# Performance work log

Hardware: AMD Instinct MI355X
Metric: run time of the kernel (lower is better)

The kernel has to match this reference:

```python
import jax, jax.numpy as jnp
import numpy as np
import math

B, T, E = 2, 2048, 1024
H = 16
D = E // H  # head_dim = 64

def setup_inputs() -> dict:
    key = jax.random.key(0)
    k1, k2, k3, k4, k5 = jax.random.split(key, 5)
    s = 0.02
    return {
        "x": jax.random.normal(k1, (B, T, E), dtype=jnp.float32),
        "W_attn": jax.random.normal(k2, (E, 3 * E), dtype=jnp.float32) * s,
        "b_attn": jax.random.normal(k3, (3 * E,), dtype=jnp.float32) * s,
        "W_proj": jax.random.normal(k4, (E, E), dtype=jnp.float32) * s,
        "b_proj": jax.random.normal(k5, (E,), dtype=jnp.float32) * s,
    }

def reference(x, W_attn, b_attn, W_proj, b_proj):
    Bx, Tx, Ex = x.shape
    qkv = x @ W_attn + b_attn                      # [B,T,3E]
    q, k, v = jnp.split(qkv, 3, axis=2)
    # [B,T,E] -> [B,H,T,D]
    def heads(t):
        return t.reshape(Bx, Tx, H, D).transpose(0, 2, 1, 3)
    q, k, v = heads(q), heads(k), heads(v)
    scores = jnp.einsum('bhqd,bhkd->bhqk', q, k) / math.sqrt(D)
    causal = jnp.tril(jnp.ones((Tx, Tx), dtype=bool))
    scores = jnp.where(causal, scores, -jnp.inf)
    attn = jax.nn.softmax(scores, axis=-1)
    out = jnp.einsum('bhqk,bhkd->bhqd', attn, v)   # [B,H,T,D]
    out = out.transpose(0, 2, 1, 3).reshape(Bx, Tx, Ex)
    return out @ W_proj + b_proj
```

## Files before the change

kernel.cpp:

```cpp
#include <hip/hip_runtime.h>


typedef unsigned short u16;
typedef unsigned int u32;
typedef __bf16 bf8 __attribute__((ext_vector_type(8)));
typedef float f32x4 __attribute__((ext_vector_type(4)));
typedef float f32x16 __attribute__((ext_vector_type(16)));
typedef u32 u32x4v __attribute__((ext_vector_type(4)));

__device__ __forceinline__ u16 f2b(float f) {
    return __builtin_bit_cast(u16, (__bf16)f);
}

__device__ __forceinline__ u32 pk2(float lo, float hi) {
    return (u32)f2b(lo) | ((u32)f2b(hi) << 16);
}

__device__ __forceinline__ f32x4 mfma16(bf8 a, bf8 b, f32x4 c) {
    return __builtin_amdgcn_mfma_f32_16x16x32_bf16(a, b, c, 0, 0, 0);
}

__device__ __forceinline__ f32x16 mfma32(bf8 a, bf8 b, f32x16 c) {
    return __builtin_amdgcn_mfma_f32_32x32x16_bf16(a, b, c, 0, 0, 0);
}

__device__ __forceinline__ float fexp2(float x) {
    return __builtin_amdgcn_exp2f(x);
}

__device__ __forceinline__ void pl32swap(u32& a, u32& b) {
    asm("v_permlane32_swap_b32 %0, %1" : "+v"(a), "+v"(b));
}

__device__ __forceinline__ void gload_lds16(const u16* g, u16* l) {
    __builtin_amdgcn_global_load_lds(
        (__attribute__((address_space(1))) void*)(g),
        (__attribute__((address_space(3))) void*)(l), 16, 0, 0);
}

__global__ __launch_bounds__(256) void k_prep(const float* __restrict__ x,
                                              const float* __restrict__ Wa,
                                              const float* __restrict__ Wp,
                                              u16* __restrict__ Xb,
                                              u16* __restrict__ WtA,
                                              u16* __restrict__ WtP) {
    __shared__ float tile[64][65];
    int id = blockIdx.x, t = threadIdx.x;
    if (id < 4096) {
        int i = id * 256 + t;
        float4 v = ((const float4*)x)[i];
        ushort4 o;
        o.x = f2b(v.x); o.y = f2b(v.y); o.z = f2b(v.z); o.w = f2b(v.w);
        ((ushort4*)Xb)[i] = o;
        return;
    }
    const float* in; u16* out; int N, j;
    if (id < 4864) { j = id - 4096; in = Wa; out = WtA; N = 3072; }
    else           { j = id - 4864; in = Wp; out = WtP; N = 1024; }
    int k0 = (j & 15) * 64, n0 = (j >> 4) * 64;
    int c = t & 63, r0 = t >> 6;
#pragma unroll
    for (int i = 0; i < 16; ++i) {
        int r = r0 + i * 4;
        tile[r][c] = in[(size_t)(k0 + r) * N + n0 + c];
    }
    __syncthreads();
#pragma unroll
    for (int i = 0; i < 16; ++i) {
        int r = r0 + i * 4;
        out[(size_t)(n0 + r) * 1024 + k0 + c] = f2b(tile[c][r]);
    }
}

#define GEMM_STAGE(GA0, GA1, GB0, GB1, K, B)                                   \
    do {                                                                       \
        gload_lds16(GA0 + (K), As[B] + tid * 8);                               \
        gload_lds16(GA1 + (K), As[B] + (256 + tid) * 8);                       \
        gload_lds16(GB0 + (K), Bs[B] + tid * 8);                               \
        gload_lds16(GB1 + (K), Bs[B] + (256 + tid) * 8);                       \
    } while (0)

#define GEMM_CORE(Aptr, Bptr)                                                  \
    int tid = threadIdx.x;                                                     \
    int w = tid >> 6, lane = tid & 63, l16 = lane & 15, quad = lane >> 4;      \
    int m0 = blockIdx.x * 128, n0 = blockIdx.y * 128;                          \
    int wr = (w >> 1) * 64, wc = (w & 1) * 64;                                 \
    __shared__ u16 As[2][128 * 32];                                            \
    __shared__ u16 Bs[2][128 * 32];                                            \
    f32x4 acc[4][4];                                                           \
    _Pragma("unroll") for (int mi = 0; mi < 4; ++mi)                           \
        _Pragma("unroll") for (int ni = 0; ni < 4; ++ni)                       \
            _Pragma("unroll") for (int r = 0; r < 4; ++r) acc[mi][ni][r] = 0.f;\
    int srow0 = tid >> 2, srow1 = 64 + srow0;                                  \
    int slc = ((tid & 3) ^ ((tid >> 3) & 3)) * 8;      \
    const u16* gA0 = Aptr + (size_t)(m0 + srow0) * 1024 + slc;                 \
    const u16* gA1 = Aptr + (size_t)(m0 + srow1) * 1024 + slc;                 \
    const u16* gB0 = Bptr + (size_t)(n0 + srow0) * 1024 + slc;                 \
    const u16* gB1 = Bptr + (size_t)(n0 + srow1) * 1024 + slc;                 \
    int cq = (quad ^ ((l16 >> 1) & 3)) * 8;               \
    GEMM_STAGE(gA0, gA1, gB0, gB1, 0, 0);                                      \
    for (int it = 0; it < 32; ++it) {                                          \
        int pb = it & 1;                                                       \
        __syncthreads();                           \
        bf8 af[4], bf[4];                                                      \
        _Pragma("unroll") for (int mi = 0; mi < 4; ++mi)                       \
            af[mi] = *(const bf8*)(As[pb] + (wr + mi * 16 + l16) * 32 + cq);   \
        _Pragma("unroll") for (int ni = 0; ni < 4; ++ni)                       \
            bf[ni] = *(const bf8*)(Bs[pb] + (wc + ni * 16 + l16) * 32 + cq);   \
        if (it < 31) GEMM_STAGE(gA0, gA1, gB0, gB1, (it + 1) * 32, pb ^ 1);    \
        _Pragma("unroll") for (int mi = 0; mi < 4; ++mi)                       \
            _Pragma("unroll") for (int ni = 0; ni < 4; ++ni)                   \
                acc[mi][ni] = mfma16(af[mi], bf[ni], acc[mi][ni]);             \
    }

__global__ __launch_bounds__(256, 3) void k_qkv(const u16* __restrict__ Xb,
                                                const u16* __restrict__ WtA,
                                                const float* __restrict__ ba,
                                                u16* __restrict__ Qb,
                                                u16* __restrict__ Kb,
                                                u16* __restrict__ Vtb) {
    GEMM_CORE(Xb, WtA)
    int sel = n0 >> 10;
    u16* dst = sel == 0 ? Qb : (sel == 1 ? Kb : Vtb);
    const float qs = 0.18033688011112042f;
#pragma unroll
    for (int ni = 0; ni < 4; ++ni) {
        int n = n0 + wc + ni * 16 + l16;
        float bias = ba[n];
        int h = (n & 1023) >> 6;
        int d = n & 63;
#pragma unroll
        for (int mi = 0; mi < 4; ++mi)
#pragma unroll
            for (int r = 0; r < 4; ++r) {
                int m = m0 + wr + mi * 16 + quad * 4 + r;
                int bb = m >> 11, tt = m & 2047;
                float v = acc[mi][ni][r] + bias;
                size_t hb = (size_t)(bb * 16 + h);
                if (sel == 2)
                    dst[hb * 131072 + (size_t)(tt >> 6) * 4096 + d * 64 + (tt & 63)] = f2b(v);
                else
                    dst[(hb * 2048 + tt) * 64 + d] =
                        f2b(sel == 0 ? v * qs : v);
            }
    }
}

__global__ __launch_bounds__(256, 3) void k_proj(const u16* __restrict__ AO,
                                                 const u16* __restrict__ WtP,
                                                 const float* __restrict__ bp,
                                                 float* __restrict__ out) {
    GEMM_CORE(AO, WtP)
#pragma unroll
    for (int ni = 0; ni < 4; ++ni) {
        int n = n0 + wc + ni * 16 + l16;
        float bias = bp[n];
#pragma unroll
        for (int mi = 0; mi < 4; ++mi)
#pragma unroll
            for (int r = 0; r < 4; ++r) {
                int m = m0 + wr + mi * 16 + quad * 4 + r;
                out[(size_t)m * 1024 + n] = acc[mi][ni][r] + bias;
            }
    }
}


#define STAGE128(KT2, B) do {                                                 \
    const u16* kt_ = Kh + (size_t)(KT2) * 8192;                               \
    const u16* vt_ = Vh + (size_t)(KT2) * 8192;                               \
    _Pragma("unroll") for (int i_ = 0; i_ < 2; ++i_) {                        \
        int ci_ = i_ * 512 + tid;             \
        gload_lds16(kt_ + (ci_ >> 3) * 64 +                                   \
                    (((ci_ & 7) ^ ((ci_ >> 3) & 7)) * 8),                     \
                    SMEM[B][0] + ci_ * 8);                                    \
        gload_lds16(vt_ + (ci_ >> 3) * 64 +                                   \
                    (((ci_ & 7) ^ ((ci_ >> 3) & 7)) * 8),                     \
                    SMEM[B][1] + ci_ * 8);                                    \
    }                                                                         \
} while (0)

#define PVSTEP(SG, BFR) do {                                                  \
    bf8 va_ = *(const bf8*)(vb_ + l31 * 64 + (((2 * (SG) + h) ^ swz) * 8));   \
    bf8 vc_ = *(const bf8*)(vb_ + (32 + l31) * 64 +                           \
                            (((2 * (SG) + h) ^ swz) * 8));                    \
    bf8 pf_ = __builtin_bit_cast(bf8, BFR);                                   \
    oT0 = mfma32(va_, pf_, oT0);                                              \
    oT1 = mfma32(vc_, pf_, oT1);                                              \
} while (0)

#define REPACK_PV(ST, SG0, SG1) do {                                          \
    u32 pk_[8];                                                               \
    _Pragma("unroll") for (int j = 0; j < 8; ++j)                             \
        pk_[j] = pk2(ST[2 * j], ST[2 * j + 1]);                               \
    pl32swap(pk_[0], pk_[2]); pl32swap(pk_[1], pk_[3]);                       \
    pl32swap(pk_[4], pk_[6]); pl32swap(pk_[5], pk_[7]);                       \
    u32x4v f0_ = {pk_[0], pk_[1], pk_[2], pk_[3]};                            \
    u32x4v f1_ = {pk_[4], pk_[5], pk_[6], pk_[7]};                            \
    PVSTEP(SG0, f0_);                                                         \
    PVSTEP(SG1, f1_);                                                         \
} while (0)

#define TREE16(S)                                                             \
    (((((S)[0] + (S)[1]) + ((S)[2] + (S)[3])) +                               \
      (((S)[4] + (S)[5]) + ((S)[6] + (S)[7]))) +                              \
     ((((S)[8] + (S)[9]) + ((S)[10] + (S)[11])) +                             \
      (((S)[12] + (S)[13]) + ((S)[14] + (S)[15]))))

__global__ __launch_bounds__(512, 4) void k_attn(const u16* __restrict__ Qb,
                                                 const u16* __restrict__ Kb,
                                                 const u16* __restrict__ Vtb,
                                                 u16* __restrict__ AO) {
    int id = blockIdx.x;
    int bh = (id & 7) * 4 + ((id >> 3) & 3);
    int t  = 15 - (id >> 5);
    int tid = threadIdx.x;
    int w = tid >> 6, lane = tid & 63, l31 = lane & 31, h = lane >> 5;
    int wq = w & 3, p = w >> 2;

    const u16* Qh = Qb  + (size_t)bh * 131072;
    const u16* Kh = Kb  + (size_t)bh * 131072;
    const u16* Vh = Vtb + (size_t)bh * 131072;

    __shared__ u16 SMEM[2][2][8192];

    int tq = 4 * t + wq;
    int qr = tq * 32;
    int ktmax = tq >> 1;
    int nk2 = t + 1;

    bf8 qf[4];
#pragma unroll
    for (int s = 0; s < 4; ++s)
        qf[s] = *(const bf8*)(Qh + (size_t)(qr + l31) * 64 + s * 16 + h * 8);

    float l_acc = 0.f;
    f32x16 oT0, oT1;
#pragma unroll
    for (int r = 0; r < 16; ++r) { oT0[r] = 0.f; oT1[r] = 0.f; }

    int swz = l31 & 7;

    STAGE128(0, 0);
    for (int k2 = 0; k2 < nk2; ++k2) {
        int pb = k2 & 1;
        __syncthreads();
        if (k2 + 1 < nk2) STAGE128(k2 + 1, pb ^ 1);

        int kt = 2 * k2 + p;
        if (kt <= ktmax) {
            const u16* kb_ = SMEM[pb][0] + p * 4096;
            const u16* vb_ = SMEM[pb][1] + p * 4096;
            bool diag = (kt == ktmax);
            bool doK1 = !(diag && ((tq & 1) == 0));

            f32x16 sT0, sT1;
#pragma unroll
            for (int r = 0; r < 16; ++r) { sT0[r] = 0.f; sT1[r] = 0.f; }
#pragma unroll
            for (int d = 0; d < 4; ++d) {
                bf8 kf = *(const bf8*)(kb_ + l31 * 64 +
                                       (((2 * d + h) ^ swz) * 8));
                sT0 = mfma32(kf, qf[d], sT0);
            }
            if (doK1) {
#pragma unroll
                for (int d = 0; d < 4; ++d) {
                    bf8 kf = *(const bf8*)(kb_ + (32 + l31) * 64 +
                                           (((2 * d + h) ^ swz) * 8));
                    sT1 = mfma32(kf, qf[d], sT1);
                }
            }

            int kb0 = kt * 64, qg = qr + l31;
            if (diag) {
#pragma unroll
                for (int r = 0; r < 16; ++r) {
                    int krow = kb0 + (r & 3) + 8 * (r >> 2) + 4 * h;
                    sT0[r] = fexp2(krow <= qg ? sT0[r] : -1e30f);
                }
                if (doK1) {
#pragma unroll
                    for (int r = 0; r < 16; ++r) {
                        int krow = kb0 + 32 + (r & 3) + 8 * (r >> 2) + 4 * h;
                        sT1[r] = fexp2(krow <= qg ? sT1[r] : -1e30f);
                    }
                }
            } else {
#pragma unroll
                for (int r = 0; r < 16; ++r) sT0[r] = fexp2(sT0[r]);
#pragma unroll
                for (int r = 0; r < 16; ++r) sT1[r] = fexp2(sT1[r]);
            }
            l_acc += TREE16(sT0);
            if (doK1) l_acc += TREE16(sT1);

            REPACK_PV(sT0, 0, 1);
            if (doK1) REPACK_PV(sT1, 2, 3);
        }
    }

    __syncthreads();
    float* comb = (float*)&SMEM[0][0][0];
    if (p == 1) {
        float* cw = comb + (wq * 64 + lane) * 36;
#pragma unroll
        for (int r = 0; r < 16; ++r) { cw[r] = oT0[r]; cw[16 + r] = oT1[r]; }
        cw[32] = l_acc;
    }
    __syncthreads();
    if (p == 1) return;

    const float* cr = comb + (wq * 64 + lane) * 36;
#pragma unroll
    for (int r = 0; r < 16; ++r) { oT0[r] += cr[r]; oT1[r] += cr[16 + r]; }
    l_acc += cr[32];

    float lsum = l_acc + __shfl_xor(l_acc, 32, 64);
    float linv = __builtin_amdgcn_rcpf(lsum);

    u32* Ot = (u32*)&SMEM[0][0][0] + 9216 + wq * 1152;
#pragma unroll
    for (int j = 0; j < 8; ++j) {
        int col = 4 * (j >> 1) + 2 * h + (j & 1);
        Ot[l31 * 36 + col]      = pk2(oT0[2 * j] * linv, oT0[2 * j + 1] * linv);
        Ot[l31 * 36 + 16 + col] = pk2(oT1[2 * j] * linv, oT1[2 * j + 1] * linv);
    }
    asm volatile("s_waitcnt lgkmcnt(0)" ::: "memory");
    __builtin_amdgcn_sched_barrier(0);

    int q2 = lane >> 1, half = lane & 1;
    int eb = bh >> 4, eh = bh & 15;
    size_t row = (size_t)eb * 2048 + qr + q2;
    const u32* src = Ot + q2 * 36 + half * 16;
    u32* dstg = (u32*)(AO + row * 1024 + eh * 64) + half * 16;
#pragma unroll
    for (int c = 0; c < 4; ++c)
        *(u32x4v*)(dstg + 4 * c) = *(const u32x4v*)(src + 4 * c);
}

extern "C" void kernel_launch(void* const* d_in, const int* in_sizes, int n_in,
                              void* d_out, int out_size, void* d_ws, size_t ws_size,
                              hipStream_t stream) {
    const float* x  = (const float*)d_in[0];
    const float* Wa = (const float*)d_in[1];
    const float* ba = (const float*)d_in[2];
    const float* Wp = (const float*)d_in[3];
    const float* bp = (const float*)d_in[4];
    float* out = (float*)d_out;

    char* ws = (char*)d_ws;
    const size_t MB = 1024 * 1024;
    u16* Xb  = (u16*)(ws);
    u16* WtA = (u16*)(ws + 8  * MB);
    u16* WtP = (u16*)(ws + 14 * MB);
    u16* Qb  = (u16*)(ws + 16 * MB);
    u16* Kb  = (u16*)(ws + 24 * MB);
    u16* Vtb = (u16*)(ws + 32 * MB);
    u16* AO  = Xb;

    k_prep<<<dim3(5120),    dim3(256), 0, stream>>>(x, Wa, Wp, Xb, WtA, WtP);
    k_qkv <<<dim3(32, 24),  dim3(256), 0, stream>>>(Xb, WtA, ba, Qb, Kb, Vtb);
    k_attn<<<dim3(512),     dim3(512), 0, stream>>>(Qb, Kb, Vtb, AO);
    k_proj<<<dim3(32, 8),   dim3(256), 0, stream>>>(AO, WtP, bp, out);
}
```

Before: 173.3 us.

## Process two query tiles per wave to reuse K/V fragments in attention

The attention block drops from 8 to 4 waves, and each wave now handles two 32-row query tiles (A and B). K and V fragments are loaded from LDS once per key tile and shared by both query tiles, which cuts LDS read traffic per MFMA. The cost is higher register pressure (two sets of accumulators and preloaded V fragments), fewer waves per block, and occupancy changed to launch_bounds(256,2). Staging and the final combine/write are adapted to the new wave mapping.

```diff
diff --git a/kernel.cpp b/kernel.cpp
--- a/kernel.cpp
+++ b/kernel.cpp
@@ -169,8 +169,8 @@
 #define STAGE128(KT2, B) do {                                                 \
     const u16* kt_ = Kh + (size_t)(KT2) * 8192;                               \
     const u16* vt_ = Vh + (size_t)(KT2) * 8192;                               \
-    _Pragma("unroll") for (int i_ = 0; i_ < 2; ++i_) {                        \
-        int ci_ = i_ * 512 + tid;             \
+    _Pragma("unroll") for (int i_ = 0; i_ < 4; ++i_) {                        \
+        int ci_ = i_ * 256 + tid;             \
         gload_lds16(kt_ + (ci_ >> 3) * 64 +                                   \
                     (((ci_ & 7) ^ ((ci_ >> 3) & 7)) * 8),                     \
                     SMEM[B][0] + ci_ * 8);                                    \
@@ -180,16 +180,13 @@
     }                                                                         \
 } while (0)
 
-#define PVSTEP(SG, BFR) do {                                                  \
-    bf8 va_ = *(const bf8*)(vb_ + l31 * 64 + (((2 * (SG) + h) ^ swz) * 8));   \
-    bf8 vc_ = *(const bf8*)(vb_ + (32 + l31) * 64 +                           \
-                            (((2 * (SG) + h) ^ swz) * 8));                    \
+#define PVSTEP(SG, BFR, O0, O1) do {                                          \
     bf8 pf_ = __builtin_bit_cast(bf8, BFR);                                   \
-    oT0 = mfma32(va_, pf_, oT0);                                              \
-    oT1 = mfma32(vc_, pf_, oT1);                                              \
+    O0 = mfma32(vfl[SG], pf_, O0);                                            \
+    O1 = mfma32(vfh[SG], pf_, O1);                                            \
 } while (0)
 
-#define REPACK_PV(ST, SG0, SG1) do {                                          \
+#define REPACK_PV(ST, SG0, SG1, O0, O1) do {                                  \
     u32 pk_[8];                                                               \
     _Pragma("unroll") for (int j = 0; j < 8; ++j)                             \
         pk_[j] = pk2(ST[2 * j], ST[2 * j + 1]);                               \
@@ -197,8 +194,8 @@
     pl32swap(pk_[4], pk_[6]); pl32swap(pk_[5], pk_[7]);                       \
     u32x4v f0_ = {pk_[0], pk_[1], pk_[2], pk_[3]};                            \
     u32x4v f1_ = {pk_[4], pk_[5], pk_[6], pk_[7]};                            \
-    PVSTEP(SG0, f0_);                                                         \
-    PVSTEP(SG1, f1_);                                                         \
+    PVSTEP(SG0, f0_, O0, O1);                                                 \
+    PVSTEP(SG1, f1_, O0, O1);                                                 \
 } while (0)
 
 #define TREE16(S)                                                             \
@@ -207,7 +204,38 @@
      ((((S)[8] + (S)[9]) + ((S)[10] + (S)[11])) +                             \
       (((S)[12] + (S)[13]) + ((S)[14] + (S)[15]))))
 
-__global__ __launch_bounds__(512, 4) void k_attn(const u16* __restrict__ Qb,
+#define TILE_BODY(QF, QR, DIAG, USEK1, LACC, O0, O1) do {                     \
+    f32x16 sT0, sT1;                                                          \
+    _Pragma("unroll") for (int r = 0; r < 16; ++r) { sT0[r] = 0.f; sT1[r] = 0.f; } \
+    _Pragma("unroll") for (int d = 0; d < 4; ++d)                             \
+        sT0 = mfma32(kf0[d], QF[d], sT0);                                     \
+    if (USEK1) {                                                              \
+        _Pragma("unroll") for (int d = 0; d < 4; ++d)                         \
+            sT1 = mfma32(kf1[d], QF[d], sT1);                                 \
+    }                                                                         \
+    int qg_ = (QR) + l31;                                                     \
+    if (DIAG) {                                                               \
+        _Pragma("unroll") for (int r = 0; r < 16; ++r) {                      \
+            int krow = kb0 + (r & 3) + 8 * (r >> 2) + 4 * h;                  \
+            sT0[r] = fexp2(krow <= qg_ ? sT0[r] : -1e30f);                    \
+        }                                                                     \
+        if (USEK1) {                                                          \
+            _Pragma("unroll") for (int r = 0; r < 16; ++r) {                  \
+                int krow = kb0 + 32 + (r & 3) + 8 * (r >> 2) + 4 * h;         \
+                sT1[r] = fexp2(krow <= qg_ ? sT1[r] : -1e30f);                \
+            }                                                                 \
+        }                                                                     \
+    } else {                                                                  \
+        _Pragma("unroll") for (int r = 0; r < 16; ++r) sT0[r] = fexp2(sT0[r]);\
+        _Pragma("unroll") for (int r = 0; r < 16; ++r) sT1[r] = fexp2(sT1[r]);\
+    }                                                                         \
+    LACC += TREE16(sT0);                                                      \
+    if (USEK1) LACC += TREE16(sT1);                                           \
+    REPACK_PV(sT0, 0, 1, O0, O1);                                             \
+    if (USEK1) REPACK_PV(sT1, 2, 3, O0, O1);                                  \
+} while (0)
+
+__global__ __launch_bounds__(256, 2) void k_attn(const u16* __restrict__ Qb,
                                                  const u16* __restrict__ Kb,
                                                  const u16* __restrict__ Vtb,
                                                  u16* __restrict__ AO) {
@@ -216,7 +244,7 @@
     int t  = 15 - (id >> 5);
     int tid = threadIdx.x;
     int w = tid >> 6, lane = tid & 63, l31 = lane & 31, h = lane >> 5;
-    int wq = w & 3, p = w >> 2;
+    int a = w & 1, p = w >> 1;
 
     const u16* Qh = Qb  + (size_t)bh * 131072;
     const u16* Kh = Kb  + (size_t)bh * 131072;
@@ -224,20 +252,25 @@
 
     __shared__ u16 SMEM[2][2][8192];
 
-    int tq = 4 * t + wq;
-    int qr = tq * 32;
-    int ktmax = tq >> 1;
+    int tqA = 4 * t + a, tqB = tqA + 2;
+    int qrA = tqA * 32, qrB = tqB * 32;
+    int ktA = 2 * t, ktB = 2 * t + 1;
     int nk2 = t + 1;
-
-    bf8 qf[4];
-#pragma unroll
-    for (int s = 0; s < 4; ++s)
-        qf[s] = *(const bf8*)(Qh + (size_t)(qr + l31) * 64 + s * 16 + h * 8);
-
-    float l_acc = 0.f;
-    f32x16 oT0, oT1;
-#pragma unroll
-    for (int r = 0; r < 16; ++r) { oT0[r] = 0.f; oT1[r] = 0.f; }
+    bool odd = (a == 1);
+
+    bf8 qfA[4], qfB[4];
+#pragma unroll
+    for (int s = 0; s < 4; ++s) {
+        qfA[s] = *(const bf8*)(Qh + (size_t)(qrA + l31) * 64 + s * 16 + h * 8);
+        qfB[s] = *(const bf8*)(Qh + (size_t)(qrB + l31) * 64 + s * 16 + h * 8);
+    }
+
+    float lA = 0.f, lB = 0.f;
+    f32x16 oA0, oA1, oB0, oB1;
+#pragma unroll
+    for (int r = 0; r < 16; ++r) {
+        oA0[r] = 0.f; oA1[r] = 0.f; oB0[r] = 0.f; oB1[r] = 0.f;
+    }
 
     int swz = l31 & 7;
 
@@ -248,95 +281,90 @@
         if (k2 + 1 < nk2) STAGE128(k2 + 1, pb ^ 1);
 
         int kt = 2 * k2 + p;
-        if (kt <= ktmax) {
-            const u16* kb_ = SMEM[pb][0] + p * 4096;
-            const u16* vb_ = SMEM[pb][1] + p * 4096;
-            bool diag = (kt == ktmax);
-            bool doK1 = !(diag && ((tq & 1) == 0));
-
-            f32x16 sT0, sT1;
-#pragma unroll
-            for (int r = 0; r < 16; ++r) { sT0[r] = 0.f; sT1[r] = 0.f; }
-#pragma unroll
-            for (int d = 0; d < 4; ++d) {
-                bf8 kf = *(const bf8*)(kb_ + l31 * 64 +
+        bool aAct  = (kt <= ktA);
+        bool diagA = (kt == ktA);
+        bool diagB = (kt == ktB);
+        bool useK1A = aAct && (!diagA || odd);
+        bool useK1B = (!diagB || odd);
+        const u16* kb_ = SMEM[pb][0] + p * 4096;
+        const u16* vb_ = SMEM[pb][1] + p * 4096;
+        int kb0 = kt * 64;
+
+        bf8 kf0[4], kf1[4];
+#pragma unroll
+        for (int d = 0; d < 4; ++d)
+            kf0[d] = *(const bf8*)(kb_ + l31 * 64 + (((2 * d + h) ^ swz) * 8));
+        if (useK1A || useK1B) {
+#pragma unroll
+            for (int d = 0; d < 4; ++d)
+                kf1[d] = *(const bf8*)(kb_ + (32 + l31) * 64 +
                                        (((2 * d + h) ^ swz) * 8));
-                sT0 = mfma32(kf, qf[d], sT0);
-            }
-            if (doK1) {
-#pragma unroll
-                for (int d = 0; d < 4; ++d) {
-                    bf8 kf = *(const bf8*)(kb_ + (32 + l31) * 64 +
-                                           (((2 * d + h) ^ swz) * 8));
-                    sT1 = mfma32(kf, qf[d], sT1);
-                }
-            }
-
-            int kb0 = kt * 64, qg = qr + l31;
-            if (diag) {
-#pragma unroll
-                for (int r = 0; r < 16; ++r) {
-                    int krow = kb0 + (r & 3) + 8 * (r >> 2) + 4 * h;
-                    sT0[r] = fexp2(krow <= qg ? sT0[r] : -1e30f);
-                }
-                if (doK1) {
-#pragma unroll
-                    for (int r = 0; r < 16; ++r) {
-                        int krow = kb0 + 32 + (r & 3) + 8 * (r >> 2) + 4 * h;
-                        sT1[r] = fexp2(krow <= qg ? sT1[r] : -1e30f);
-                    }
-                }
-            } else {
-#pragma unroll
-                for (int r = 0; r < 16; ++r) sT0[r] = fexp2(sT0[r]);
-#pragma unroll
-                for (int r = 0; r < 16; ++r) sT1[r] = fexp2(sT1[r]);
-            }
-            l_acc += TREE16(sT0);
-            if (doK1) l_acc += TREE16(sT1);
-
-            REPACK_PV(sT0, 0, 1);
-            if (doK1) REPACK_PV(sT1, 2, 3);
         }
+        bf8 vfl[4], vfh[4];
+#pragma unroll
+        for (int sg = 0; sg < 4; ++sg) {
+            vfl[sg] = *(const bf8*)(vb_ + l31 * 64 + (((2 * sg + h) ^ swz) * 8));
+            vfh[sg] = *(const bf8*)(vb_ + (32 + l31) * 64 +
+                                    (((2 * sg + h) ^ swz) * 8));
+        }
+
+        if (aAct) TILE_BODY(qfA, qrA, diagA, useK1A, lA, oA0, oA1);
+        TILE_BODY(qfB, qrB, diagB, useK1B, lB, oB0, oB1);
     }
 
     __syncthreads();
     float* comb = (float*)&SMEM[0][0][0];
     if (p == 1) {
-        float* cw = comb + (wq * 64 + lane) * 36;
-#pragma unroll
-        for (int r = 0; r < 16; ++r) { cw[r] = oT0[r]; cw[16 + r] = oT1[r]; }
-        cw[32] = l_acc;
+        float* cwA = comb + ((a * 2 + 0) * 64 + lane) * 36;
+        float* cwB = comb + ((a * 2 + 1) * 64 + lane) * 36;
+#pragma unroll
+        for (int r = 0; r < 16; ++r) {
+            cwA[r] = oA0[r]; cwA[16 + r] = oA1[r];
+            cwB[r] = oB0[r]; cwB[16 + r] = oB1[r];
+        }
+        cwA[32] = lA; cwB[32] = lB;
     }
     __syncthreads();
     if (p == 1) return;
 
-    const float* cr = comb + (wq * 64 + lane) * 36;
-#pragma unroll
-    for (int r = 0; r < 16; ++r) { oT0[r] += cr[r]; oT1[r] += cr[16 + r]; }
-    l_acc += cr[32];
-
-    float lsum = l_acc + __shfl_xor(l_acc, 32, 64);
-    float linv = __builtin_amdgcn_rcpf(lsum);
-
-    u32* Ot = (u32*)&SMEM[0][0][0] + 9216 + wq * 1152;
+    const float* crA = comb + ((a * 2 + 0) * 64 + lane) * 36;
+    const float* crB = comb + ((a * 2 + 1) * 64 + lane) * 36;
+#pragma unroll
+    for (int r = 0; r < 16; ++r) {
+        oA0[r] += crA[r]; oA1[r] += crA[16 + r];
+        oB0[r] += crB[r]; oB1[r] += crB[16 + r];
+    }
+    lA += crA[32]; lB += crB[32];
+
+    float lsA = lA + __shfl_xor(lA, 32, 64);
+    float lsB = lB + __shfl_xor(lB, 32, 64);
+    float livA = __builtin_amdgcn_rcpf(lsA);
+    float livB = __builtin_amdgcn_rcpf(lsB);
+
+    u32* OtA = (u32*)&SMEM[0][0][0] + 9216 + (a * 2 + 0) * 1152;
+    u32* OtB = (u32*)&SMEM[0][0][0] + 9216 + (a * 2 + 1) * 1152;
 #pragma unroll
     for (int j = 0; j < 8; ++j) {
         int col = 4 * (j >> 1) + 2 * h + (j & 1);
-        Ot[l31 * 36 + col]      = pk2(oT0[2 * j] * linv, oT0[2 * j + 1] * linv);
-        Ot[l31 * 36 + 16 + col] = pk2(oT1[2 * j] * linv, oT1[2 * j + 1] * linv);
+        OtA[l31 * 36 + col]      = pk2(oA0[2 * j] * livA, oA0[2 * j + 1] * livA);
+        OtA[l31 * 36 + 16 + col] = pk2(oA1[2 * j] * livA, oA1[2 * j + 1] * livA);
+        OtB[l31 * 36 + col]      = pk2(oB0[2 * j] * livB, oB0[2 * j + 1] * livB);
+        OtB[l31 * 36 + 16 + col] = pk2(oB1[2 * j] * livB, oB1[2 * j + 1] * livB);
     }
     asm volatile("s_waitcnt lgkmcnt(0)" ::: "memory");
     __builtin_amdgcn_sched_barrier(0);
 
     int q2 = lane >> 1, half = lane & 1;
     int eb = bh >> 4, eh = bh & 15;
-    size_t row = (size_t)eb * 2048 + qr + q2;
-    const u32* src = Ot + q2 * 36 + half * 16;
-    u32* dstg = (u32*)(AO + row * 1024 + eh * 64) + half * 16;
-#pragma unroll
-    for (int c = 0; c < 4; ++c)
-        *(u32x4v*)(dstg + 4 * c) = *(const u32x4v*)(src + 4 * c);
+    const u32* srcA = OtA + q2 * 36 + half * 16;
+    const u32* srcB = OtB + q2 * 36 + half * 16;
+    u32* dgA = (u32*)(AO + ((size_t)eb * 2048 + qrA + q2) * 1024 + eh * 64) + half * 16;
+    u32* dgB = (u32*)(AO + ((size_t)eb * 2048 + qrB + q2) * 1024 + eh * 64) + half * 16;
+#pragma unroll
+    for (int c = 0; c < 4; ++c) {
+        *(u32x4v*)(dgA + 4 * c) = *(const u32x4v*)(srcA + 4 * c);
+        *(u32x4v*)(dgB + 4 * c) = *(const u32x4v*)(srcB + 4 * c);
+    }
 }
 
 extern "C" void kernel_launch(void* const* d_in, const int* in_sizes, int n_in,
@@ -361,6 +389,6 @@
 
     k_prep<<<dim3(5120),    dim3(256), 0, stream>>>(x, Wa, Wp, Xb, WtA, WtP);
     k_qkv <<<dim3(32, 24),  dim3(256), 0, stream>>>(Xb, WtA, ba, Qb, Kb, Vtb);
-    k_attn<<<dim3(512),     dim3(512), 0, stream>>>(Qb, Kb, Vtb, AO);
+    k_attn<<<dim3(512),     dim3(256), 0, stream>>>(Qb, Kb, Vtb, AO);
     k_proj<<<dim3(32, 8),   dim3(256), 0, stream>>>(AO, WtP, bp, out);
 }
```

Result: no change. 173.8 us (+0.3%).
